# Kernel optimization log

Measured on AMD Instinct MI355X. Metric: run time of the kernel, lower is better.

Reference implementation:

```python
import jax, jax.numpy as jnp
import numpy as np

DIM = 768
HEADS = 12
HEAD_DIM = DIM // HEADS
HIDDEN = int(DIM * 4.0)
EPS = 1e-5


def layernorm(x, w, b):
    mu = jnp.mean(x, axis=-1, keepdims=True)
    var = jnp.var(x, axis=-1, keepdims=True)
    return (x - mu) * jax.lax.rsqrt(var + EPS) * w + b


def setup_inputs() -> dict:
    key = jax.random.key(0)
    ks = jax.random.split(key, 12)
    B, N = 4, 2048
    s = lambda fan_in: 1.0 / np.sqrt(fan_in)
    return {
        "x": jax.random.normal(ks[0], (B, N, DIM), dtype=jnp.float32),
        "qkv_w": jax.random.normal(ks[1], (3 * DIM, DIM), dtype=jnp.float32) * s(DIM),
        "proj_w": jax.random.normal(ks[2], (DIM, DIM), dtype=jnp.float32) * s(DIM),
        "proj_b": jnp.zeros((DIM,), dtype=jnp.float32),
        "norm1_w": jnp.ones((DIM,), dtype=jnp.float32),
        "norm1_b": jnp.zeros((DIM,), dtype=jnp.float32),
        "norm2_w": jnp.ones((DIM,), dtype=jnp.float32),
        "norm2_b": jnp.zeros((DIM,), dtype=jnp.float32),
        "fc1_w": jax.random.normal(ks[3], (HIDDEN, DIM), dtype=jnp.float32) * s(DIM),
        "fc1_b": jnp.zeros((HIDDEN,), dtype=jnp.float32),
        "fc2_w": jax.random.normal(ks[4], (DIM, HIDDEN), dtype=jnp.float32) * s(HIDDEN),
        "fc2_b": jnp.zeros((DIM,), dtype=jnp.float32),
    }


def reference(x, qkv_w, proj_w, proj_b, norm1_w, norm1_b, norm2_w, norm2_b,
              fc1_w, fc1_b, fc2_w, fc2_b):
    B, N, C = x.shape
    scale = HEAD_DIM ** -0.5
    shortcut = x
    h = layernorm(x, norm1_w, norm1_b)
    # qkv: [B, N, 3C] -> [3, B, H, N, Dh]
    qkv = (h @ qkv_w.T).reshape(B, N, 3, HEADS, HEAD_DIM)
    qkv = jnp.transpose(qkv, (2, 0, 3, 1, 4))
    q, k, v = qkv[0] * scale, qkv[1], qkv[2]
    attn = jnp.einsum("bhnd,bhmd->bhnm", q, k)
    attn = jax.nn.softmax(attn, axis=-1)
    out = jnp.einsum("bhnm,bhmd->bhnd", attn, v)
    out = jnp.transpose(out, (0, 2, 1, 3)).reshape(B, N, C)
    out = out @ proj_w.T + proj_b
    x = shortcut + out
    h2 = layernorm(x, norm2_w, norm2_b)
    mlp = jax.nn.gelu(h2 @ fc1_w.T + fc1_b, approximate=False) @ fc2_w.T + fc2_b
    return x + mlp
```

## Files before the change

### kernel.cpp

```cpp
#include <hip/hip_runtime.h>
#include <hip/hip_bf16.h>

#define SEQ   2048
#define NBAT  4
#define NH    12
#define HD    64
#define CDIM  768
#define HID   3072
#define NTOK  (SEQ*NBAT)

#define KS2 0.1803368801111244f

typedef __attribute__((ext_vector_type(8))) short short8;
typedef __attribute__((ext_vector_type(4))) float floatx4;

__device__ __forceinline__ float bf2f(unsigned short u) {
    union { unsigned int i; float f; } v; v.i = ((unsigned int)u) << 16; return v.f;
}
__device__ __forceinline__ unsigned short f2bf(float f) {
    union { float f; unsigned int i; } v; v.f = f;
    unsigned int i = v.i;
    return (unsigned short)((i + 0x7FFFu + ((i >> 16) & 1u)) >> 16);
}
__device__ __forceinline__ unsigned int fbits(float f) {
    union { float f; unsigned int i; } v; v.f = f; return v.i;
}
__device__ __forceinline__ float fast_exp2(float x) {
#if __has_builtin(__builtin_amdgcn_exp2f)
    return __builtin_amdgcn_exp2f(x);
#else
    return __expf(x * 0.69314718055994531f);
#endif
}
__device__ __forceinline__ float fast_rcp(float x) {
#if __has_builtin(__builtin_amdgcn_rcpf)
    return __builtin_amdgcn_rcpf(x);
#else
    return 1.f / x;
#endif
}
__device__ __forceinline__ float gelu_f(float v) {
    float u = 0.7978845608028654f * v * (1.f + 0.044715f * v * v);
    float e = fast_exp2(u * 2.885390081777927f);
    float th = 1.f - 2.f * fast_rcp(e + 1.f);
    return 0.5f * v * (1.f + th);
}
__device__ __forceinline__ void gload16(const unsigned short* g, unsigned short* l) {
    __builtin_amdgcn_global_load_lds(
        (const __attribute__((address_space(1))) unsigned int*)g,
        (__attribute__((address_space(3))) unsigned int*)l, 16, 0, 0);
}

__global__ __launch_bounds__(256) void cvt_all_kernel(
    const float* __restrict__ s0, const float* __restrict__ s1,
    const float* __restrict__ s2, const float* __restrict__ s3,
    unsigned short* __restrict__ d0, unsigned short* __restrict__ d1,
    unsigned short* __restrict__ d2, unsigned short* __restrict__ d3)
{
    int blk = blockIdx.x;
    const float* src; unsigned short* dst; int off;
    if (blk < 1728)      { src = s0; dst = d0; off = blk; }
    else if (blk < 2304) { src = s1; dst = d1; off = blk - 1728; }
    else if (blk < 4608) { src = s2; dst = d2; off = blk - 2304; }
    else                 { src = s3; dst = d3; off = blk - 4608; }
    int i = (off * 256 + threadIdx.x) * 4;
    float4 f = *(const float4*)(src + i);
    ushort4 o;
    o.x = f2bf(f.x); o.y = f2bf(f.y); o.z = f2bf(f.z); o.w = f2bf(f.w);
    *(ushort4*)(dst + i) = o;
}

__global__ __launch_bounds__(256) void ln_kernel(
    const float* __restrict__ x, const float* __restrict__ w,
    const float* __restrict__ b, unsigned short* __restrict__ y)
{
    int row  = blockIdx.x * 4 + (threadIdx.x >> 6);
    int lane = threadIdx.x & 63;
    const float4* xr = (const float4*)(x + (size_t)row * CDIM);
    float4 v[3];
    float s = 0.f, sq = 0.f;
#pragma unroll
    for (int i = 0; i < 3; i++) {
        float4 f = xr[lane + i * 64];
        v[i] = f;
        s  += (f.x + f.y) + (f.z + f.w);
        sq += (f.x * f.x + f.y * f.y) + (f.z * f.z + f.w * f.w);
    }
#pragma unroll
    for (int o = 32; o > 0; o >>= 1) {
        s  += __shfl_xor(s,  o, 64);
        sq += __shfl_xor(sq, o, 64);
    }
    float mean = s * (1.f / CDIM);
    float var  = sq * (1.f / CDIM) - mean * mean;
    float rstd = rsqrtf(var + 1e-5f);
    const float4* w4 = (const float4*)w;
    const float4* b4 = (const float4*)b;
    ushort4* y4 = (ushort4*)(y + (size_t)row * CDIM);
#pragma unroll
    for (int i = 0; i < 3; i++) {
        int c = lane + i * 64;
        float4 wf = w4[c], bf_ = b4[c];
        ushort4 o;
        o.x = f2bf((v[i].x - mean) * rstd * wf.x + bf_.x);
        o.y = f2bf((v[i].y - mean) * rstd * wf.y + bf_.y);
        o.z = f2bf((v[i].z - mean) * rstd * wf.z + bf_.z);
        o.w = f2bf((v[i].w - mean) * rstd * wf.w + bf_.w);
        y4[c] = o;
    }
}

#define BK 64

template<int ACT, int OUT32, int TM>
__global__ __launch_bounds__(256) void gemm_bt(
    const unsigned short* __restrict__ A, const unsigned short* __restrict__ W,
    const float* __restrict__ bias, const float* __restrict__ res,
    void* __restrict__ Cv, int M, int N, int K, int scol, float scale)
{
    constexpr int MT   = TM / 32;
    constexpr int ISSA = TM / 32;
    __shared__ __align__(16) unsigned short As[TM * BK];
    __shared__ __align__(16) unsigned short Bs[128 * BK];
    int tid  = threadIdx.x;
    int wave = tid >> 6, lane = tid & 63;
    int wr = wave >> 1, wc = wave & 1;
    int quad = lane >> 4, l15 = lane & 15;
    int m0 = blockIdx.x * TM, n0 = blockIdx.y * 128;

    int r8 = lane >> 3;
    int kc = (lane & 7) ^ r8;
    const unsigned short* Ag = A + (size_t)(m0 + wave * (TM / 4) + r8) * K + kc * 8;
    const unsigned short* Wg = W + (size_t)(n0 + wave * 32 + r8) * K + kc * 8;
    unsigned short* AsW = As + wave * (TM / 4) * BK;
    unsigned short* BsW = Bs + wave * 32 * BK;

    floatx4 acc[MT][4];
    floatx4 fz = {0.f, 0.f, 0.f, 0.f};
#pragma unroll
    for (int i = 0; i < MT; i++)
#pragma unroll
        for (int j = 0; j < 4; j++) acc[i][j] = fz;

    int sw = l15 & 7;
    for (int k0 = 0; k0 < K; k0 += BK) {
        __syncthreads();
#pragma unroll
        for (int j = 0; j < ISSA; j++)
            gload16(Ag + (size_t)(8 * j) * K + k0, AsW + j * 512);
#pragma unroll
        for (int j = 0; j < 4; j++)
            gload16(Wg + (size_t)(8 * j) * K + k0, BsW + j * 512);
        __syncthreads();

#pragma unroll
        for (int s = 0; s < 2; s++) {
            short8 af[MT], bfg[4];
            int ko = ((s * 4 + quad) ^ sw) * 8;
#pragma unroll
            for (int mt = 0; mt < MT; mt++)
                af[mt] = *(const short8*)(As + (wr * (TM / 2) + mt * 16 + l15) * BK + ko);
#pragma unroll
            for (int nt = 0; nt < 4; nt++)
                bfg[nt] = *(const short8*)(Bs + (wc * 64 + nt * 16 + l15) * BK + ko);
#pragma unroll
            for (int mt = 0; mt < MT; mt++)
#pragma unroll
                for (int nt = 0; nt < 4; nt++)
                    acc[mt][nt] = __builtin_amdgcn_mfma_f32_16x16x32_bf16(
                        af[mt], bfg[nt], acc[mt][nt], 0, 0, 0);
        }
    }

#pragma unroll
    for (int mt = 0; mt < MT; mt++) {
#pragma unroll
        for (int nt = 0; nt < 4; nt++) {
            int col = n0 + wc * 64 + nt * 16 + l15;
            float bv = bias ? bias[col] : 0.f;
            float cs = (col < scol) ? scale : 1.f;
#pragma unroll
            for (int r = 0; r < 4; r++) {
                int row = m0 + wr * (TM / 2) + mt * 16 + quad * 4 + r;
                size_t idx = (size_t)row * N + col;
                float v = acc[mt][nt][r] + bv;
                if (res) v += res[idx];
                if (ACT == 1) v = gelu_f(v);
                v *= cs;
                if (OUT32) ((float*)Cv)[idx] = v;
                else       ((unsigned short*)Cv)[idx] = f2bf(v);
            }
        }
    }
}

__global__ __launch_bounds__(256) void attn_kernel(
    const unsigned short* __restrict__ qkv, unsigned short* __restrict__ out)
{
    __shared__ __align__(16) unsigned short Ks[2][64 * 72];
    __shared__ __align__(16) unsigned short Vt[2][64 * 72];
    __shared__ __align__(16) unsigned short Ps[4][16 * 72];

    int tid  = threadIdx.x;
    int wave = tid >> 6, lane = tid & 63;
    int quad = lane >> 4, l15 = lane & 15;
    int bh = blockIdx.y;
    int b  = bh / NH, h = bh % NH;
    size_t base = (size_t)b * SEQ * 2304 + h * 64;
    int qbase = blockIdx.x * 128 + wave * 32;

    short8 bq[2][2];
#pragma unroll
    for (int qh = 0; qh < 2; qh++)
#pragma unroll
        for (int kk = 0; kk < 2; kk++)
            bq[qh][kk] = *(const short8*)(qkv + base +
                (size_t)(qbase + qh * 16 + l15) * 2304 + kk * 32 + quad * 8);

    floatx4 o[2][4];
    floatx4 fz = {0.f, 0.f, 0.f, 0.f};
#pragma unroll
    for (int qh = 0; qh < 2; qh++)
#pragma unroll
        for (int dg = 0; dg < 4; dg++) o[qh][dg] = fz;
    float m2[2]  = {-3e38f, -3e38f};
    float ls[2]  = {0.f, 0.f};

    const unsigned short* kptr = qkv + base + 768;
    const unsigned short* vptr = qkv + base + 1536;

    int skey = tid >> 2;
    int sd   = (tid & 3) * 16;
    int vj   = tid & 31;
    int vd8  = wave * 16 + ((tid >> 5) & 1) * 8;

    uint4 k0v = *(const uint4*)(kptr + (size_t)skey * 2304 + sd);
    uint4 k1v = *(const uint4*)(kptr + (size_t)skey * 2304 + sd + 8);
    uint4 v0v = *(const uint4*)(vptr + (size_t)(2 * vj)     * 2304 + vd8);
    uint4 v1v = *(const uint4*)(vptr + (size_t)(2 * vj + 1) * 2304 + vd8);

    for (int t = 0; t < SEQ / 64; t++) {
        int cur = t & 1;
        unsigned short* K_ = Ks[cur];
        unsigned short* V_ = Vt[cur];
        *(uint4*)(K_ + skey * 72 + sd)     = k0v;
        *(uint4*)(K_ + skey * 72 + sd + 8) = k1v;
        union { uint4 q; unsigned short u[8]; } u0, u1;
        u0.q = v0v; u1.q = v1v;
#pragma unroll
        for (int i = 0; i < 8; i++) {
            unsigned int w = (unsigned int)u0.u[i] | ((unsigned int)u1.u[i] << 16);
            *(unsigned int*)(V_ + (vd8 + i) * 72 + 2 * vj) = w;
        }
        __syncthreads();

        if (t + 1 < SEQ / 64) {
            int kt = (t + 1) * 64;
            k0v = *(const uint4*)(kptr + (size_t)(kt + skey) * 2304 + sd);
            k1v = *(const uint4*)(kptr + (size_t)(kt + skey) * 2304 + sd + 8);
            v0v = *(const uint4*)(vptr + (size_t)(kt + 2 * vj)     * 2304 + vd8);
            v1v = *(const uint4*)(vptr + (size_t)(kt + 2 * vj + 1) * 2304 + vd8);
        }

#pragma unroll
        for (int qh = 0; qh < 2; qh++) {
            floatx4 st[4];
#pragma unroll
            for (int ts = 0; ts < 4; ts++) {
                floatx4 s = fz;
#pragma unroll
                for (int kk = 0; kk < 2; kk++) {
                    short8 ak = *(const short8*)(K_ + (ts * 16 + l15) * 72 + kk * 32 + quad * 8);
                    s = __builtin_amdgcn_mfma_f32_16x16x32_bf16(ak, bq[qh][kk], s, 0, 0, 0);
                }
                st[ts] = s;
            }

            float tmax = st[0][0];
#pragma unroll
            for (int ts = 0; ts < 4; ts++)
#pragma unroll
                for (int r = 0; r < 4; r++) tmax = fmaxf(tmax, st[ts][r]);
            tmax = fmaxf(tmax, __shfl_xor(tmax, 16, 64));
            tmax = fmaxf(tmax, __shfl_xor(tmax, 32, 64));
            if (tmax > m2[qh]) {
                float alpha = fast_exp2(m2[qh] - tmax);
                m2[qh] = tmax;
                ls[qh] *= alpha;
#pragma unroll
                for (int dg = 0; dg < 4; dg++)
#pragma unroll
                    for (int r = 0; r < 4; r++) o[qh][dg][r] *= alpha;
            }
            float p[4][4];
            float psum = 0.f;
            float mm = m2[qh];
#pragma unroll
            for (int ts = 0; ts < 4; ts++)
#pragma unroll
                for (int r = 0; r < 4; r++) {
                    p[ts][r] = fast_exp2(st[ts][r] - mm);
                    psum += p[ts][r];
                }
            ls[qh] += psum;
#pragma unroll
            for (int ts = 0; ts < 4; ts++) {
                unsigned int w01 = __builtin_amdgcn_perm(fbits(p[ts][1]), fbits(p[ts][0]), 0x07060302);
                unsigned int w23 = __builtin_amdgcn_perm(fbits(p[ts][3]), fbits(p[ts][2]), 0x07060302);
                uint2 wv; wv.x = w01; wv.y = w23;
                *(uint2*)(Ps[wave] + l15 * 72 + ts * 16 + quad * 4) = wv;
            }

#pragma unroll
            for (int hk = 0; hk < 2; hk++) {
                short8 bp = *(const short8*)(Ps[wave] + l15 * 72 + hk * 32 + quad * 8);
#pragma unroll
                for (int dg = 0; dg < 4; dg++) {
                    short8 av = *(const short8*)(V_ + (dg * 16 + l15) * 72 + hk * 32 + quad * 8);
                    o[qh][dg] = __builtin_amdgcn_mfma_f32_16x16x32_bf16(av, bp, o[qh][dg], 0, 0, 0);
                }
            }
        }
    }

#pragma unroll
    for (int qh = 0; qh < 2; qh++) {
        float l = ls[qh];
        l += __shfl_xor(l, 16, 64);
        l += __shfl_xor(l, 32, 64);
        float inv = 1.f / l;
        size_t orow = ((size_t)b * SEQ + qbase + qh * 16 + l15) * CDIM + h * 64;
#pragma unroll
        for (int dg = 0; dg < 4; dg++) {
            unsigned int u0 = (unsigned int)f2bf(o[qh][dg][0] * inv) | ((unsigned int)f2bf(o[qh][dg][1] * inv) << 16);
            unsigned int u1 = (unsigned int)f2bf(o[qh][dg][2] * inv) | ((unsigned int)f2bf(o[qh][dg][3] * inv) << 16);
            uint2 wv; wv.x = u0; wv.y = u1;
            *(uint2*)((unsigned short*)out + orow + dg * 16 + quad * 4) = wv;
        }
    }
}

extern "C" void kernel_launch(void* const* d_in, const int* in_sizes, int n_in,
                              void* d_out, int out_size, void* d_ws, size_t ws_size,
                              hipStream_t stream)
{
    const float* x      = (const float*)d_in[0];
    const float* qkv_w  = (const float*)d_in[1];
    const float* proj_w = (const float*)d_in[2];
    const float* proj_b = (const float*)d_in[3];
    const float* n1w    = (const float*)d_in[4];
    const float* n1b    = (const float*)d_in[5];
    const float* n2w    = (const float*)d_in[6];
    const float* n2b    = (const float*)d_in[7];
    const float* fc1w   = (const float*)d_in[8];
    const float* fc1b   = (const float*)d_in[9];
    const float* fc2w   = (const float*)d_in[10];
    const float* fc2b   = (const float*)d_in[11];
    float* out = (float*)d_out;

    unsigned short* ws = (unsigned short*)d_ws;
    unsigned short* wq = ws;
    unsigned short* wp = wq + 1769472;
    unsigned short* w1 = wp + 589824;
    unsigned short* w2 = w1 + 2359296;
    unsigned short* h    = w2 + 2359296;
    unsigned short* qkv  = h + 6291456;
    unsigned short* attn = qkv + 18874368;
    unsigned short* a    = qkv;

    dim3 blk(256);
    cvt_all_kernel<<<6912, blk, 0, stream>>>(qkv_w, proj_w, fc1w, fc2w, wq, wp, w1, w2);

    ln_kernel<<<NTOK / 4, blk, 0, stream>>>(x, n1w, n1b, h);
    gemm_bt<0, 0, 128><<<dim3(NTOK / 128, 2304 / 128), blk, 0, stream>>>(
        h, wq, nullptr, nullptr, qkv, NTOK, 2304, 768, 768, KS2);
    attn_kernel<<<dim3(SEQ / 128, NBAT * NH), blk, 0, stream>>>(qkv, attn);
    gemm_bt<0, 1, 64><<<dim3(NTOK / 64, 768 / 128), blk, 0, stream>>>(
        attn, wp, proj_b, x, out, NTOK, 768, 768, 0, 1.f);
    ln_kernel<<<NTOK / 4, blk, 0, stream>>>(out, n2w, n2b, h);
    gemm_bt<1, 0, 128><<<dim3(NTOK / 128, 3072 / 128), blk, 0, stream>>>(
        h, w1, fc1b, nullptr, a, NTOK, 3072, 768, 0, 1.f);
    gemm_bt<0, 1, 64><<<dim3(NTOK / 64, 768 / 128), blk, 0, stream>>>(
        a, w2, fc2b, out, out, NTOK, 768, 3072, 0, 1.f);
}
```

Baseline: 407.0 us.

## Async-load K tiles into swizzled LDS and share K/V fragments across query halves

The attention kernel now loads K tiles straight from global memory into LDS with gload16, using an XOR-swizzled unpadded layout, instead of staging them through registers. Each K and V fragment is read from LDS once and used for both query halves, and P gets a separate buffer per half so the PV MFMAs for both halves can be interleaved. The V transpose store for the next tile is moved after the compute, leaving a single barrier per iteration. The aim is less LDS traffic, fewer register round-trips and better overlap of global loads with MFMA work, at the cost of more live registers for the doubled score tiles.

```diff
diff --git a/kernel.cpp b/kernel.cpp
--- a/kernel.cpp
+++ b/kernel.cpp
@@ -197,9 +197,9 @@
 __global__ __launch_bounds__(256) void attn_kernel(
     const unsigned short* __restrict__ qkv, unsigned short* __restrict__ out)
 {
-    __shared__ __align__(16) unsigned short Ks[2][64 * 72];
+    __shared__ __align__(16) unsigned short Ks[2][64 * 64];
     __shared__ __align__(16) unsigned short Vt[2][64 * 72];
-    __shared__ __align__(16) unsigned short Ps[4][16 * 72];
+    __shared__ __align__(16) unsigned short Ps[4][2][16 * 72];
 
     int tid  = threadIdx.x;
     int wave = tid >> 6, lane = tid & 63;
@@ -223,64 +223,63 @@
     for (int qh = 0; qh < 2; qh++)
 #pragma unroll
         for (int dg = 0; dg < 4; dg++) o[qh][dg] = fz;
-    float m2[2]  = {-3e38f, -3e38f};
-    float ls[2]  = {0.f, 0.f};
-
-    const unsigned short* kptr = qkv + base + 768;
+    float m2[2] = {-3e38f, -3e38f};
+    float ls[2] = {0.f, 0.f};
+
+    const unsigned short* kg = qkv + base + 768 +
+        (size_t)(wave * 16 + (lane >> 3)) * 2304 + (((lane & 7) ^ ((lane >> 3) & 7)) * 8);
     const unsigned short* vptr = qkv + base + 1536;
-
-    int skey = tid >> 2;
-    int sd   = (tid & 3) * 16;
-    int vj   = tid & 31;
-    int vd8  = wave * 16 + ((tid >> 5) & 1) * 8;
-
-    uint4 k0v = *(const uint4*)(kptr + (size_t)skey * 2304 + sd);
-    uint4 k1v = *(const uint4*)(kptr + (size_t)skey * 2304 + sd + 8);
-    uint4 v0v = *(const uint4*)(vptr + (size_t)(2 * vj)     * 2304 + vd8);
-    uint4 v1v = *(const uint4*)(vptr + (size_t)(2 * vj + 1) * 2304 + vd8);
-
-    for (int t = 0; t < SEQ / 64; t++) {
-        int cur = t & 1;
-        unsigned short* K_ = Ks[cur];
-        unsigned short* V_ = Vt[cur];
-        *(uint4*)(K_ + skey * 72 + sd)     = k0v;
-        *(uint4*)(K_ + skey * 72 + sd + 8) = k1v;
+    int vj  = tid & 31;
+    int vd8 = wave * 16 + ((tid >> 5) & 1) * 8;
+    int sw  = l15 & 7;
+
+    gload16(kg, &Ks[0][wave * 1024]);
+    gload16(kg + (size_t)8 * 2304, &Ks[0][wave * 1024 + 512]);
+    {
+        uint4 v0v = *(const uint4*)(vptr + (size_t)(2 * vj)     * 2304 + vd8);
+        uint4 v1v = *(const uint4*)(vptr + (size_t)(2 * vj + 1) * 2304 + vd8);
         union { uint4 q; unsigned short u[8]; } u0, u1;
         u0.q = v0v; u1.q = v1v;
 #pragma unroll
         for (int i = 0; i < 8; i++) {
             unsigned int w = (unsigned int)u0.u[i] | ((unsigned int)u1.u[i] << 16);
-            *(unsigned int*)(V_ + (vd8 + i) * 72 + 2 * vj) = w;
-        }
-        __syncthreads();
-
-        if (t + 1 < SEQ / 64) {
+            *(unsigned int*)(&Vt[0][(vd8 + i) * 72 + 2 * vj]) = w;
+        }
+    }
+    __syncthreads();
+
+    for (int t = 0; t < SEQ / 64; t++) {
+        int cur = t & 1, nxt = cur ^ 1;
+        bool more = (t + 1 < SEQ / 64);
+        uint4 v0v, v1v;
+        if (more) {
+            const unsigned short* kg2 = kg + (size_t)(t + 1) * 64 * 2304;
+            gload16(kg2, &Ks[nxt][wave * 1024]);
+            gload16(kg2 + (size_t)8 * 2304, &Ks[nxt][wave * 1024 + 512]);
             int kt = (t + 1) * 64;
-            k0v = *(const uint4*)(kptr + (size_t)(kt + skey) * 2304 + sd);
-            k1v = *(const uint4*)(kptr + (size_t)(kt + skey) * 2304 + sd + 8);
             v0v = *(const uint4*)(vptr + (size_t)(kt + 2 * vj)     * 2304 + vd8);
             v1v = *(const uint4*)(vptr + (size_t)(kt + 2 * vj + 1) * 2304 + vd8);
         }
 
+        floatx4 st[2][4];
+#pragma unroll
+        for (int ts = 0; ts < 4; ts++) {
+            short8 ak0 = *(const short8*)(&Ks[cur][(ts * 16 + l15) * 64 + (((0 * 4 + quad) ^ sw) * 8)]);
+            short8 ak1 = *(const short8*)(&Ks[cur][(ts * 16 + l15) * 64 + (((1 * 4 + quad) ^ sw) * 8)]);
+            floatx4 s0 = __builtin_amdgcn_mfma_f32_16x16x32_bf16(ak0, bq[0][0], fz, 0, 0, 0);
+            s0 = __builtin_amdgcn_mfma_f32_16x16x32_bf16(ak1, bq[0][1], s0, 0, 0, 0);
+            floatx4 s1 = __builtin_amdgcn_mfma_f32_16x16x32_bf16(ak0, bq[1][0], fz, 0, 0, 0);
+            s1 = __builtin_amdgcn_mfma_f32_16x16x32_bf16(ak1, bq[1][1], s1, 0, 0, 0);
+            st[0][ts] = s0; st[1][ts] = s1;
+        }
+
 #pragma unroll
         for (int qh = 0; qh < 2; qh++) {
-            floatx4 st[4];
-#pragma unroll
-            for (int ts = 0; ts < 4; ts++) {
-                floatx4 s = fz;
-#pragma unroll
-                for (int kk = 0; kk < 2; kk++) {
-                    short8 ak = *(const short8*)(K_ + (ts * 16 + l15) * 72 + kk * 32 + quad * 8);
-                    s = __builtin_amdgcn_mfma_f32_16x16x32_bf16(ak, bq[qh][kk], s, 0, 0, 0);
-                }
-                st[ts] = s;
-            }
-
-            float tmax = st[0][0];
+            float tmax = st[qh][0][0];
 #pragma unroll
             for (int ts = 0; ts < 4; ts++)
 #pragma unroll
-                for (int r = 0; r < 4; r++) tmax = fmaxf(tmax, st[ts][r]);
+                for (int r = 0; r < 4; r++) tmax = fmaxf(tmax, st[qh][ts][r]);
             tmax = fmaxf(tmax, __shfl_xor(tmax, 16, 64));
             tmax = fmaxf(tmax, __shfl_xor(tmax, 32, 64));
             if (tmax > m2[qh]) {
@@ -292,35 +291,45 @@
 #pragma unroll
                     for (int r = 0; r < 4; r++) o[qh][dg][r] *= alpha;
             }
-            float p[4][4];
+            float mm = m2[qh];
             float psum = 0.f;
-            float mm = m2[qh];
-#pragma unroll
-            for (int ts = 0; ts < 4; ts++)
-#pragma unroll
-                for (int r = 0; r < 4; r++) {
-                    p[ts][r] = fast_exp2(st[ts][r] - mm);
-                    psum += p[ts][r];
-                }
+#pragma unroll
+            for (int ts = 0; ts < 4; ts++) {
+                float p0 = fast_exp2(st[qh][ts][0] - mm);
+                float p1 = fast_exp2(st[qh][ts][1] - mm);
+                float p2 = fast_exp2(st[qh][ts][2] - mm);
+                float p3 = fast_exp2(st[qh][ts][3] - mm);
+                psum += (p0 + p1) + (p2 + p3);
+                unsigned int w01 = __builtin_amdgcn_perm(fbits(p1), fbits(p0), 0x07060302);
+                unsigned int w23 = __builtin_amdgcn_perm(fbits(p3), fbits(p2), 0x07060302);
+                uint2 wv; wv.x = w01; wv.y = w23;
+                *(uint2*)(&Ps[wave][qh][l15 * 72 + ts * 16 + quad * 4]) = wv;
+            }
             ls[qh] += psum;
-#pragma unroll
-            for (int ts = 0; ts < 4; ts++) {
-                unsigned int w01 = __builtin_amdgcn_perm(fbits(p[ts][1]), fbits(p[ts][0]), 0x07060302);
-                unsigned int w23 = __builtin_amdgcn_perm(fbits(p[ts][3]), fbits(p[ts][2]), 0x07060302);
-                uint2 wv; wv.x = w01; wv.y = w23;
-                *(uint2*)(Ps[wave] + l15 * 72 + ts * 16 + quad * 4) = wv;
-            }
-
-#pragma unroll
-            for (int hk = 0; hk < 2; hk++) {
-                short8 bp = *(const short8*)(Ps[wave] + l15 * 72 + hk * 32 + quad * 8);
-#pragma unroll
-                for (int dg = 0; dg < 4; dg++) {
-                    short8 av = *(const short8*)(V_ + (dg * 16 + l15) * 72 + hk * 32 + quad * 8);
-                    o[qh][dg] = __builtin_amdgcn_mfma_f32_16x16x32_bf16(av, bp, o[qh][dg], 0, 0, 0);
-                }
-            }
-        }
+        }
+
+#pragma unroll
+        for (int hk = 0; hk < 2; hk++) {
+            short8 bp0 = *(const short8*)(&Ps[wave][0][l15 * 72 + hk * 32 + quad * 8]);
+            short8 bp1 = *(const short8*)(&Ps[wave][1][l15 * 72 + hk * 32 + quad * 8]);
+#pragma unroll
+            for (int dg = 0; dg < 4; dg++) {
+                short8 av = *(const short8*)(&Vt[cur][(dg * 16 + l15) * 72 + hk * 32 + quad * 8]);
+                o[0][dg] = __builtin_amdgcn_mfma_f32_16x16x32_bf16(av, bp0, o[0][dg], 0, 0, 0);
+                o[1][dg] = __builtin_amdgcn_mfma_f32_16x16x32_bf16(av, bp1, o[1][dg], 0, 0, 0);
+            }
+        }
+
+        if (more) {
+            union { uint4 q; unsigned short u[8]; } u0, u1;
+            u0.q = v0v; u1.q = v1v;
+#pragma unroll
+            for (int i = 0; i < 8; i++) {
+                unsigned int w = (unsigned int)u0.u[i] | ((unsigned int)u1.u[i] << 16);
+                *(unsigned int*)(&Vt[nxt][(vd8 + i) * 72 + 2 * vj]) = w;
+            }
+        }
+        __syncthreads();
     }
 
 #pragma unroll
```

After: 393.2 us. 1.04x faster.
